# Performance work log

Measured on AMD Instinct MI355X. Metric: run time of the kernel, lower is better.

Reference implementation:

```python
import jax, jax.numpy as jnp
import numpy as np

B, N, C_IN, C_H, C_OUT, R, X_DIM = 32, 256, 64, 128, 128, 5, 1024
NEG = -9e15

def _leaky(x, s=0.2):
    return jnp.where(x >= 0, x, s * x)

def gat_layer(atoms, mask, W, b, a):
    # atoms: (B,n,c_in), mask: (B,n,n,R) bool, W: (c_in, R*c), b: (R*c,), a: (R, 2c)
    bs, n, _ = atoms.shape
    c = a.shape[1] // 2
    h = (atoms @ W + b).reshape(bs, n, R, c)            # (B,n,R,c)
    src = jnp.einsum('bnrc,rc->bnr', h, a[:, :c])       # a . h_i part
    dst = jnp.einsum('bnrc,rc->bnr', h, a[:, c:])       # a . h_j part
    logits = _leaky(src[:, :, None, :] + dst[:, None, :, :])  # (B,i,j,R)
    masked = jnp.where(mask, logits, NEG)
    probs = jax.nn.softmax(masked.reshape(bs, n, n * R), axis=2).reshape(bs, n, n, R)
    return jnp.einsum('bijr,bjrc->bic', probs, h)       # (B,n,c)

def setup_inputs() -> dict:
    key = jax.random.key(0)
    ks = jax.random.split(key, 16)
    def p(k, shape, fan):
        return jax.random.normal(k, shape, jnp.float32) * (1.414 / np.sqrt(fan))
    inp = {
        'x': jax.random.normal(ks[0], (B, X_DIM), jnp.float32),
        'y_atoms': jax.random.normal(ks[1], (B, N, C_IN), jnp.float32),
        'y_bonds': jax.random.randint(ks[2], (B, N, N, R), 0, 2, jnp.int32),
        'W1': p(ks[3], (C_IN, R * C_H), C_IN), 'b1': jnp.zeros((R * C_H,), jnp.float32),
        'a1': p(ks[4], (R, 2 * C_H), 2 * C_H),
        'W2': p(ks[5], (C_H, R * C_H), C_H), 'b2': jnp.zeros((R * C_H,), jnp.float32),
        'a2': p(ks[6], (R, 2 * C_H), 2 * C_H),
        'W3': p(ks[7], (C_H, R * C_OUT), C_H), 'b3': jnp.zeros((R * C_OUT,), jnp.float32),
        'a3': p(ks[8], (R, 2 * C_OUT), 2 * C_OUT),
        'We1': p(ks[9], (2 * C_OUT + X_DIM, 256), 2 * C_OUT + X_DIM), 'be1': jnp.zeros((256,), jnp.float32),
        'We2': p(ks[10], (256, 32), 256), 'be2': jnp.zeros((32,), jnp.float32),
        'We3': p(ks[11], (32, 1), 32), 'be3': jnp.zeros((1,), jnp.float32),
    }
    return inp

def reference(x, y_atoms, y_bonds, W1, b1, a1, W2, b2, a2, W3, b3, a3,
              We1, be1, We2, be2, We3, be3):
    mask = (y_bonds == 1)
    h = gat_layer(y_atoms, mask, W1, b1, a1)
    h = _leaky(h)                                   # dropout is identity at eval
    h = gat_layer(h, mask, W2, b2, a2)
    h = _leaky(h)
    h = gat_layer(h, mask, W3, b3, a3)
    y_feats = jnp.concatenate([jnp.mean(h, axis=1), jnp.max(h, axis=1)], axis=1)
    z = jnp.concatenate([x, y_feats], axis=1)
    z = _leaky(z @ We1 + be1)
    z = _leaky(z @ We2 + be2)
    return z @ We3 + be3
```

## Files before the change

### kernel.cpp

```cpp
#include <hip/hip_runtime.h>
#include <cstddef>

#define BB 32
#define NN 256
#define RR 5

typedef __attribute__((ext_vector_type(8))) short bf16x8;
typedef __attribute__((ext_vector_type(4))) float f32x4;

__device__ __forceinline__ float lrelu(float x) { return x >= 0.f ? x : 0.2f * x; }
__device__ __forceinline__ unsigned short f2bf(float x) {
    unsigned u = __float_as_uint(x);
    u += 0x7FFFu + ((u >> 16) & 1u);
    return (unsigned short)(u >> 16);
}
__device__ __forceinline__ float bf2f(unsigned short u) {
    return __uint_as_float((unsigned)u << 16);
}

__global__ __launch_bounds__(256) void k_prep(const float* __restrict__ W1,
                                              const float* __restrict__ W2,
                                              const float* __restrict__ W3,
                                              const int* __restrict__ bonds,
                                              unsigned short* __restrict__ WT1,
                                              unsigned short* __restrict__ WT2,
                                              unsigned short* __restrict__ WT3,
                                              unsigned char* __restrict__ maskp) {
    int blk = blockIdx.x;
    int t = threadIdx.x;
    if (blk < 30) {
        int layer = blk / 10, nt = blk % 10;
        const float* W;
        unsigned short* WT;
        int K;
        if (layer == 0)      { W = W1; WT = WT1; K = 64; }
        else if (layer == 1) { W = W2; WT = WT2; K = 128; }
        else                 { W = W3; WT = WT3; K = 128; }
        int n = nt * 64 + (t & 63);
        for (int kg = (int)(t >> 6); kg < K / 8; kg += 4) {
            bf16x8 v;
#pragma unroll
            for (int e = 0; e < 8; ++e) v[e] = (short)f2bf(W[(size_t)(kg * 8 + e) * 640 + n]);
            *(bf16x8*)&WT[(size_t)n * K + kg * 8] = v;
        }
    } else {
        int gt = (blk - 30) * 256 + t;
        const int4* p = (const int4*)(bonds + (size_t)gt * 20);
        int4 q0 = p[0], q1 = p[1], q2 = p[2], q3 = p[3], q4 = p[4];
        int v[20] = {q0.x, q0.y, q0.z, q0.w, q1.x, q1.y, q1.z, q1.w,
                     q2.x, q2.y, q2.z, q2.w, q3.x, q3.y, q3.z, q3.w,
                     q4.x, q4.y, q4.z, q4.w};
        unsigned m = 0;
#pragma unroll
        for (int k = 0; k < 4; ++k)
#pragma unroll
            for (int r = 0; r < 5; ++r)
                m |= (v[k * 5 + r] == 1) ? (1u << (k * 8 + r)) : 0u;
        *(unsigned*)&maskp[(size_t)gt * 4] = m;
    }
}

template <int K, int MODE>
__global__ __launch_bounds__(256) void k_gemm_h(const float* __restrict__ Af32,
                                                const unsigned short* __restrict__ Ab,
                                                const unsigned short* __restrict__ WTg,
                                                const float* __restrict__ bias,
                                                const float* __restrict__ avec,
                                                float* __restrict__ srcp,
                                                float* __restrict__ dstp,
                                                unsigned short* __restrict__ hTf) {
    const int t = threadIdx.x;
    const int l = blockIdx.x;
    const int mt = (l & 7) * 16 + ((l >> 3) & 15);
    const int nt = l >> 7;
    const int n0 = nt * 64, m0 = mt * 64;
    const int w = t >> 6, lane = t & 63;
    const int colg = lane & 15, rquad = lane >> 4;
    const int m = m0 + w * 16 + colg;
    const int koff = rquad * 8;

    f32x4 acc[4] = {};
#pragma unroll
    for (int kk = 0; kk < K; kk += 32) {
        bf16x8 af;
        size_t off = (size_t)m * K + kk + koff;
        if (MODE == 1) {
            af = *(const bf16x8*)&Ab[off];
        } else {
            float4 q0 = *(const float4*)&Af32[off];
            float4 q1 = *(const float4*)&Af32[off + 4];
            af[0] = (short)f2bf(q0.x); af[1] = (short)f2bf(q0.y);
            af[2] = (short)f2bf(q0.z); af[3] = (short)f2bf(q0.w);
            af[4] = (short)f2bf(q1.x); af[5] = (short)f2bf(q1.y);
            af[6] = (short)f2bf(q1.z); af[7] = (short)f2bf(q1.w);
        }
#pragma unroll
        for (int ct = 0; ct < 4; ++ct) {
            bf16x8 bfv = *(const bf16x8*)&WTg[(size_t)(n0 + ct * 16 + colg) * K + kk + koff];
            acc[ct] = __builtin_amdgcn_mfma_f32_16x16x32_bf16(af, bfv, acc[ct], 0, 0, 0);
        }
    }

    const int r = n0 >> 7, chalf = n0 & 127;
    const int b = m0 >> 8, jb = m0 & 255;
    float val[4][4];
    float ssum[4] = {0.f, 0.f, 0.f, 0.f}, dsum[4] = {0.f, 0.f, 0.f, 0.f};
#pragma unroll
    for (int ct = 0; ct < 4; ++ct) {
        int cg = chalf + ct * 16 + colg;
        float bv = bias[n0 + ct * 16 + colg];
        float asr = avec[r * 256 + cg];
        float ads = avec[r * 256 + 128 + cg];
#pragma unroll
        for (int reg = 0; reg < 4; ++reg) {
            float v = acc[ct][reg] + bv;
            val[ct][reg] = v;
            ssum[reg] += v * asr;
            dsum[reg] += v * ads;
        }
    }
#pragma unroll
    for (int mk = 1; mk < 16; mk <<= 1)
#pragma unroll
        for (int reg = 0; reg < 4; ++reg) {
            ssum[reg] += __shfl_xor(ssum[reg], mk);
            dsum[reg] += __shfl_xor(dsum[reg], mk);
        }
    if (colg == 0) {
        int half = (n0 >> 6) & 1;
#pragma unroll
        for (int reg = 0; reg < 4; ++reg) {
            int row = m0 + w * 16 + rquad * 4 + reg;
            srcp[half * 40960 + row * 5 + r] = ssum[reg];
            dstp[half * 40960 + row * 5 + r] = dsum[reg];
        }
    }
    {
        const int joct = (jb >> 3) + w * 2 + (rquad >> 1);
        const size_t tile = (size_t)((b * 5 + r) * 32 + joct) * 1024;
        const int sub = (rquad & 1) * 4;
#pragma unroll
        for (int ct = 0; ct < 4; ++ct) {
            int c = chalf + ct * 16 + colg;
            uint2 pk;
            pk.x = (unsigned)f2bf(val[ct][0]) | ((unsigned)f2bf(val[ct][1]) << 16);
            pk.y = (unsigned)f2bf(val[ct][2]) | ((unsigned)f2bf(val[ct][3]) << 16);
            *(uint2*)&hTf[tile + (size_t)c * 8 + sub] = pk;
        }
    }
}

template <int FINAL>
__global__ __launch_bounds__(512, 4) void k_agg(const unsigned short* __restrict__ hTf,
                                                const float* __restrict__ srcp,
                                                const float* __restrict__ dstp,
                                                const unsigned char* __restrict__ maskp,
                                                unsigned short* __restrict__ Ab,
                                                float* __restrict__ poolS,
                                                float* __restrict__ poolM) {
    __shared__ __align__(16) unsigned short Ps[20480];
    __shared__ __align__(16) float Ds2l[1280];
    __shared__ float Ss[80], Zw[128], Zrow[16];
    const int t = threadIdx.x;
    const int l = blockIdx.x;
    const int b = (l & 7) * 4 + ((l >> 3) & 3);
    const int itile = l >> 5;
    const int ib = b * 256 + itile * 16;
    const int w = t >> 6, lane = t & 63;
    const int colg = lane & 15, rquad = lane >> 4;
    const int c = w * 16 + colg;
    const size_t bbase = (size_t)(b * 5) * 32 * 1024;

    if (t < 80) Ss[t] = srcp[(size_t)ib * 5 + t] + srcp[40960 + (size_t)ib * 5 + t];
    for (int idx = t; idx < 1280; idx += 512) {
        int jl = idx & 255, rr = idx >> 8;
        size_t o = (size_t)(b * 256 + jl) * 5 + rr;
        Ds2l[rr * 256 + jl] = dstp[o] + dstp[40960 + o];
    }
    bf16x8 pre[4];
#pragma unroll
    for (int s = 0; s < 4; ++s)
        pre[s] = *(const bf16x8*)&hTf[bbase + (size_t)(s * 4 + rquad) * 1024 + (size_t)c * 8];
    __syncthreads();

    {
        const int i = t & 15;
        const int kq = (t >> 4) & 3;
        float esum = 0.f;
#pragma unroll
        for (int it = 0; it < 5; ++it) {
            int p = it * 512 + t;
            int s = p >> 6;
            int k0 = s * 32 + kq * 8;
            int rr = k0 >> 8, j0 = k0 & 255;
            uint2 mk8 = *(const uint2*)&maskp[((size_t)(ib + i) << 8) + j0];
            float sv = Ss[i * 5 + rr];
            float4 d0 = *(const float4*)&Ds2l[rr * 256 + j0];
            float4 d1 = *(const float4*)&Ds2l[rr * 256 + j0 + 4];
            float dv[8] = {d0.x, d0.y, d0.z, d0.w, d1.x, d1.y, d1.z, d1.w};
            bf16x8 pv;
#pragma unroll
            for (int e = 0; e < 8; ++e) {
                unsigned mb = ((e < 4 ? (mk8.x >> (8 * e)) : (mk8.y >> (8 * (e - 4)))) >> rr) & 1u;
                float vv = lrelu(sv + dv[e]);
                float ev = mb ? __expf(vv) : 0.f;
                unsigned short q = f2bf(ev);
                pv[e] = (short)q;
                esum += __uint_as_float((unsigned)q << 16);
            }
            *(bf16x8*)&Ps[p * 8] = pv;
        }
        esum += __shfl_xor(esum, 16);
        esum += __shfl_xor(esum, 32);
        if (lane < 16) Zw[w * 16 + (lane & 15)] = esum;
    }
    __syncthreads();
    if (t < 16) {
        float z = 0.f;
#pragma unroll
        for (int ww = 0; ww < 8; ++ww) z += Zw[ww * 16 + t];
        Zrow[t] = 1.f / z;
    }

    f32x4 acc0 = {}, acc1 = {};
#pragma unroll
    for (int s = 0; s < 8; ++s) {
        bf16x8 af = *(const bf16x8*)&Ps[(s * 64 + lane) * 8];
        bf16x8 bfv;
        if (s < 4) bfv = pre[s];
        else bfv = *(const bf16x8*)&hTf[bbase + (size_t)((s & 7) * 4 + rquad) * 1024 + (size_t)c * 8];
        if (s & 1) acc1 = __builtin_amdgcn_mfma_f32_16x16x32_bf16(af, bfv, acc1, 0, 0, 0);
        else       acc0 = __builtin_amdgcn_mfma_f32_16x16x32_bf16(af, bfv, acc0, 0, 0, 0);
    }
#pragma unroll 8
    for (int s = 8; s < 40; ++s) {
        bf16x8 af = *(const bf16x8*)&Ps[(s * 64 + lane) * 8];
        bf16x8 bfv = *(const bf16x8*)&hTf[bbase +
            (size_t)((s >> 3) * 32 + (s & 7) * 4 + rquad) * 1024 + (size_t)c * 8];
        if (s & 1) acc1 = __builtin_amdgcn_mfma_f32_16x16x32_bf16(af, bfv, acc1, 0, 0, 0);
        else       acc0 = __builtin_amdgcn_mfma_f32_16x16x32_bf16(af, bfv, acc0, 0, 0, 0);
    }
    __syncthreads();
    const int irow = ib + rquad * 4;
    if (FINAL) {
        float ps = 0.f, pm = -3.4e38f;
#pragma unroll
        for (int reg = 0; reg < 4; ++reg) {
            float v = (acc0[reg] + acc1[reg]) * Zrow[rquad * 4 + reg];
            ps += v;
            pm = fmaxf(pm, v);
        }
        ps += __shfl_xor(ps, 16);
        ps += __shfl_xor(ps, 32);
        pm = fmaxf(pm, __shfl_xor(pm, 16));
        pm = fmaxf(pm, __shfl_xor(pm, 32));
        if (rquad == 0) {
            poolS[(size_t)(b * 16 + itile) * 128 + c] = ps;
            poolM[(size_t)(b * 16 + itile) * 128 + c] = pm;
        }
    } else {
#pragma unroll
        for (int reg = 0; reg < 4; ++reg) {
            float v = (acc0[reg] + acc1[reg]) * Zrow[rquad * 4 + reg];
            Ab[(size_t)(irow + reg) * 128 + c] = f2bf(lrelu(v));
        }
    }
}

__global__ __launch_bounds__(256) void k_mlp1(const float* __restrict__ x,
                                              const float* __restrict__ poolS,
                                              const float* __restrict__ poolM,
                                              const float* __restrict__ We1,
                                              float* __restrict__ z1p) {
    const int kg = blockIdx.x, b = blockIdx.y;
    const int t = threadIdx.x;
    __shared__ float zs[256];
    if (kg < 4) {
        zs[t] = x[(size_t)b * 1024 + kg * 256 + t];
    } else if (t < 128) {
        float s = 0.f;
#pragma unroll
        for (int it = 0; it < 16; ++it) s += poolS[(size_t)(b * 16 + it) * 128 + t];
        zs[t] = s * (1.f / 256.f);
    } else {
        int f = t - 128;
        float mx = -3.4e38f;
#pragma unroll
        for (int it = 0; it < 16; ++it) mx = fmaxf(mx, poolM[(size_t)(b * 16 + it) * 128 + f]);
        zs[t] = mx;
    }
    __syncthreads();
    float s = 0.f;
#pragma unroll 8
    for (int k = 0; k < 256; ++k) s += zs[k] * We1[(size_t)(kg * 256 + k) * 256 + t];
    z1p[(size_t)(b * 5 + kg) * 256 + t] = s;
}

__global__ __launch_bounds__(256) void k_mlp2(const float* __restrict__ z1p,
                                              const float* __restrict__ be1,
                                              const float* __restrict__ We2,
                                              const float* __restrict__ be2,
                                              const float* __restrict__ We3,
                                              const float* __restrict__ be3,
                                              float* __restrict__ out) {
    const int b = blockIdx.x, t = threadIdx.x;
    __shared__ float z1s[256];
    __shared__ float s2p[8][32];
    __shared__ float z2s[32];
    {
        float s = be1[t];
#pragma unroll
        for (int kg = 0; kg < 5; ++kg) s += z1p[(size_t)(b * 5 + kg) * 256 + t];
        z1s[t] = lrelu(s);
    }
    __syncthreads();
    {
        int o = t & 31, g = t >> 5;
        float p = 0.f;
#pragma unroll
        for (int k = 0; k < 32; ++k) p += z1s[g * 32 + k] * We2[(g * 32 + k) * 32 + o];
        s2p[g][o] = p;
    }
    __syncthreads();
    if (t < 32) {
        float s2 = be2[t];
#pragma unroll
        for (int g = 0; g < 8; ++g) s2 += s2p[g][t];
        z2s[t] = lrelu(s2);
    }
    __syncthreads();
    if (t == 0) {
        float s3 = be3[0];
#pragma unroll
        for (int k = 0; k < 32; ++k) s3 += z2s[k] * We3[k];
        out[b] = s3;
    }
}

constexpr size_t O_MASK  = 0;
constexpr size_t O_SRCP  = 2097152;
constexpr size_t O_DSTP  = O_SRCP + 2ull * 40960 * 4;
constexpr size_t O_AB    = O_DSTP + 2ull * 40960 * 4;
constexpr size_t O_HT    = O_AB + 2097152;
constexpr size_t O_WT1   = O_HT + 5242880ull * 2;
constexpr size_t O_WT2   = O_WT1 + 640ull * 64 * 2;
constexpr size_t O_WT3   = O_WT2 + 640ull * 128 * 2;
constexpr size_t O_POOLS = O_WT3 + 640ull * 128 * 2;
constexpr size_t O_POOLM = O_POOLS + 32ull * 16 * 128 * 4;
constexpr size_t O_Z1P   = O_POOLM + 32ull * 16 * 128 * 4;

extern "C" void kernel_launch(void* const* d_in, const int* in_sizes, int n_in,
                              void* d_out, int out_size, void* d_ws, size_t ws_size,
                              hipStream_t stream) {
    const float* x       = (const float*)d_in[0];
    const float* y_atoms = (const float*)d_in[1];
    const int*   y_bonds = (const int*)d_in[2];
    const float* W1 = (const float*)d_in[3];
    const float* b1 = (const float*)d_in[4];
    const float* a1 = (const float*)d_in[5];
    const float* W2 = (const float*)d_in[6];
    const float* b2 = (const float*)d_in[7];
    const float* a2 = (const float*)d_in[8];
    const float* W3 = (const float*)d_in[9];
    const float* b3 = (const float*)d_in[10];
    const float* a3 = (const float*)d_in[11];
    const float* We1 = (const float*)d_in[12];
    const float* be1 = (const float*)d_in[13];
    const float* We2 = (const float*)d_in[14];
    const float* be2 = (const float*)d_in[15];
    const float* We3 = (const float*)d_in[16];
    const float* be3 = (const float*)d_in[17];
    float* out = (float*)d_out;

    char* ws = (char*)d_ws;
    unsigned char* maskp = (unsigned char*)(ws + O_MASK);
    float* srcp = (float*)(ws + O_SRCP);
    float* dstp = (float*)(ws + O_DSTP);
    unsigned short* Ab = (unsigned short*)(ws + O_AB);
    unsigned short* hTf = (unsigned short*)(ws + O_HT);
    unsigned short* WT1 = (unsigned short*)(ws + O_WT1);
    unsigned short* WT2 = (unsigned short*)(ws + O_WT2);
    unsigned short* WT3 = (unsigned short*)(ws + O_WT3);
    float* poolS = (float*)(ws + O_POOLS);
    float* poolM = (float*)(ws + O_POOLM);
    float* z1p   = (float*)(ws + O_Z1P);

    dim3 blk(256);

    k_prep<<<2078, blk, 0, stream>>>(W1, W2, W3, y_bonds, WT1, WT2, WT3, maskp);

    k_gemm_h<64, 0><<<1280, blk, 0, stream>>>(
        y_atoms, nullptr, WT1, b1, a1, srcp, dstp, hTf);
    k_agg<0><<<512, dim3(512), 0, stream>>>(hTf, srcp, dstp, maskp, Ab, nullptr, nullptr);

    k_gemm_h<128, 1><<<1280, blk, 0, stream>>>(
        nullptr, Ab, WT2, b2, a2, srcp, dstp, hTf);
    k_agg<0><<<512, dim3(512), 0, stream>>>(hTf, srcp, dstp, maskp, Ab, nullptr, nullptr);

    k_gemm_h<128, 1><<<1280, blk, 0, stream>>>(
        nullptr, Ab, WT3, b3, a3, srcp, dstp, hTf);
    k_agg<1><<<512, dim3(512), 0, stream>>>(hTf, srcp, dstp, maskp, nullptr, poolS, poolM);

    k_mlp1<<<dim3(5, 32), blk, 0, stream>>>(x, poolS, poolM, We1, z1p);
    k_mlp2<<<32, blk, 0, stream>>>(z1p, be1, We2, be2, We3, be3, out);
}
```

Measured before the change: 202.1 us.

## Fuse all stages into one persistent kernel with atomic grid barriers

Replaces the nine separate launches (prep, three GEMM/aggregation pairs, two MLP stages) with a single persistent kernel of 512 blocks of 512 threads. Stages are separated by software grid barriers built on an atomic counter. Each block runs two 256-thread GEMM sub-tiles at once, and the W2/W3 transposes and mask packing are overlapped with the first GEMM stage. The aim is to remove per-launch overhead and tail gaps between kernels. In exchange it adds barrier spin cost and a memset, and it depends on all 512 blocks being co-resident, otherwise it deadlocks.

```diff
diff --git a/kernel.cpp b/kernel.cpp
--- a/kernel.cpp
+++ b/kernel.cpp
@@ -1,9 +1,7 @@
 #include <hip/hip_runtime.h>
 #include <cstddef>
 
-#define BB 32
-#define NN 256
-#define RR 5
+#define NBLK 512
 
 typedef __attribute__((ext_vector_type(8))) short bf16x8;
 typedef __attribute__((ext_vector_type(4))) float f32x4;
@@ -18,59 +16,56 @@
     return __uint_as_float((unsigned)u << 16);
 }
 
-__global__ __launch_bounds__(256) void k_prep(const float* __restrict__ W1,
-                                              const float* __restrict__ W2,
-                                              const float* __restrict__ W3,
-                                              const int* __restrict__ bonds,
-                                              unsigned short* __restrict__ WT1,
-                                              unsigned short* __restrict__ WT2,
-                                              unsigned short* __restrict__ WT3,
-                                              unsigned char* __restrict__ maskp) {
-    int blk = blockIdx.x;
-    int t = threadIdx.x;
-    if (blk < 30) {
-        int layer = blk / 10, nt = blk % 10;
-        const float* W;
-        unsigned short* WT;
-        int K;
-        if (layer == 0)      { W = W1; WT = WT1; K = 64; }
-        else if (layer == 1) { W = W2; WT = WT2; K = 128; }
-        else                 { W = W3; WT = WT3; K = 128; }
-        int n = nt * 64 + (t & 63);
-        for (int kg = (int)(t >> 6); kg < K / 8; kg += 4) {
-            bf16x8 v;
-#pragma unroll
-            for (int e = 0; e < 8; ++e) v[e] = (short)f2bf(W[(size_t)(kg * 8 + e) * 640 + n]);
-            *(bf16x8*)&WT[(size_t)n * K + kg * 8] = v;
-        }
-    } else {
-        int gt = (blk - 30) * 256 + t;
-        const int4* p = (const int4*)(bonds + (size_t)gt * 20);
-        int4 q0 = p[0], q1 = p[1], q2 = p[2], q3 = p[3], q4 = p[4];
-        int v[20] = {q0.x, q0.y, q0.z, q0.w, q1.x, q1.y, q1.z, q1.w,
-                     q2.x, q2.y, q2.z, q2.w, q3.x, q3.y, q3.z, q3.w,
-                     q4.x, q4.y, q4.z, q4.w};
-        unsigned m = 0;
-#pragma unroll
-        for (int k = 0; k < 4; ++k)
-#pragma unroll
-            for (int r = 0; r < 5; ++r)
-                m |= (v[k * 5 + r] == 1) ? (1u << (k * 8 + r)) : 0u;
-        *(unsigned*)&maskp[(size_t)gt * 4] = m;
-    }
+__device__ __forceinline__ void gbar(unsigned* bar, unsigned target) {
+    __syncthreads();
+    if (threadIdx.x == 0) {
+        __threadfence();
+        __hip_atomic_fetch_add(bar, 1u, __ATOMIC_RELAXED, __HIP_MEMORY_SCOPE_AGENT);
+        while (__hip_atomic_load(bar, __ATOMIC_RELAXED, __HIP_MEMORY_SCOPE_AGENT) < target)
+            __builtin_amdgcn_s_sleep(8);
+        __threadfence();
+    }
+    __syncthreads();
+}
+
+__device__ __forceinline__ void wtrans(const float* __restrict__ W,
+                                       unsigned short* __restrict__ WT,
+                                       int K, int nt, int t) {
+    int n = nt * 64 + (t & 63);
+    for (int kg = t >> 6; kg < K / 8; kg += 8) {
+        bf16x8 v;
+#pragma unroll
+        for (int e = 0; e < 8; ++e) v[e] = (short)f2bf(W[(size_t)(kg * 8 + e) * 640 + n]);
+        *(bf16x8*)&WT[(size_t)n * K + kg * 8] = v;
+    }
+}
+
+__device__ __forceinline__ void maskpack(const int* __restrict__ bonds,
+                                         unsigned char* __restrict__ maskp, int gt) {
+    const int4* p = (const int4*)(bonds + (size_t)gt * 20);
+    int4 q0 = p[0], q1 = p[1], q2 = p[2], q3 = p[3], q4 = p[4];
+    int v[20] = {q0.x, q0.y, q0.z, q0.w, q1.x, q1.y, q1.z, q1.w,
+                 q2.x, q2.y, q2.z, q2.w, q3.x, q3.y, q3.z, q3.w,
+                 q4.x, q4.y, q4.z, q4.w};
+    unsigned m = 0;
+#pragma unroll
+    for (int k = 0; k < 4; ++k)
+#pragma unroll
+        for (int r = 0; r < 5; ++r)
+            m |= (v[k * 5 + r] == 1) ? (1u << (k * 8 + r)) : 0u;
+    *(unsigned*)&maskp[(size_t)gt * 4] = m;
 }
 
 template <int K, int MODE>
-__global__ __launch_bounds__(256) void k_gemm_h(const float* __restrict__ Af32,
-                                                const unsigned short* __restrict__ Ab,
-                                                const unsigned short* __restrict__ WTg,
-                                                const float* __restrict__ bias,
-                                                const float* __restrict__ avec,
-                                                float* __restrict__ srcp,
-                                                float* __restrict__ dstp,
-                                                unsigned short* __restrict__ hTf) {
-    const int t = threadIdx.x;
-    const int l = blockIdx.x;
+__device__ __forceinline__ void gemm_body(int l, int t,
+                                          const float* __restrict__ Af32,
+                                          const unsigned short* __restrict__ Ab,
+                                          const unsigned short* __restrict__ WTg,
+                                          const float* __restrict__ bias,
+                                          const float* __restrict__ avec,
+                                          float* __restrict__ srcp,
+                                          float* __restrict__ dstp,
+                                          unsigned short* __restrict__ hTf) {
     const int mt = (l & 7) * 16 + ((l >> 3) & 15);
     const int nt = l >> 7;
     const int n0 = nt * 64, m0 = mt * 64;
@@ -127,12 +122,12 @@
             dsum[reg] += __shfl_xor(dsum[reg], mk);
         }
     if (colg == 0) {
-        int half = (n0 >> 6) & 1;
+        int nhalf = (n0 >> 6) & 1;
 #pragma unroll
         for (int reg = 0; reg < 4; ++reg) {
             int row = m0 + w * 16 + rquad * 4 + reg;
-            srcp[half * 40960 + row * 5 + r] = ssum[reg];
-            dstp[half * 40960 + row * 5 + r] = dsum[reg];
+            srcp[nhalf * 40960 + row * 5 + r] = ssum[reg];
+            dstp[nhalf * 40960 + row * 5 + r] = dsum[reg];
         }
     }
     {
@@ -151,18 +146,20 @@
 }
 
 template <int FINAL>
-__global__ __launch_bounds__(512, 4) void k_agg(const unsigned short* __restrict__ hTf,
-                                                const float* __restrict__ srcp,
-                                                const float* __restrict__ dstp,
-                                                const unsigned char* __restrict__ maskp,
-                                                unsigned short* __restrict__ Ab,
-                                                float* __restrict__ poolS,
-                                                float* __restrict__ poolM) {
-    __shared__ __align__(16) unsigned short Ps[20480];
-    __shared__ __align__(16) float Ds2l[1280];
-    __shared__ float Ss[80], Zw[128], Zrow[16];
-    const int t = threadIdx.x;
-    const int l = blockIdx.x;
+__device__ __forceinline__ void agg_body(int l, int t, unsigned char* SM,
+                                         const unsigned short* __restrict__ hTf,
+                                         const float* __restrict__ srcp,
+                                         const float* __restrict__ dstp,
+                                         const unsigned char* __restrict__ maskp,
+                                         unsigned short* __restrict__ Ab,
+                                         float* __restrict__ poolS,
+                                         float* __restrict__ poolM) {
+    unsigned short* Ps = (unsigned short*)SM;
+    float* Ds2l = (float*)(SM + 40960);
+    float* Ss   = (float*)(SM + 46080);
+    float* Zw   = (float*)(SM + 46400);
+    float* Zrow = (float*)(SM + 46912);
+
     const int b = (l & 7) * 4 + ((l >> 3) & 3);
     const int itile = l >> 5;
     const int ib = b * 256 + itile * 16;
@@ -267,14 +264,13 @@
     }
 }
 
-__global__ __launch_bounds__(256) void k_mlp1(const float* __restrict__ x,
-                                              const float* __restrict__ poolS,
-                                              const float* __restrict__ poolM,
-                                              const float* __restrict__ We1,
-                                              float* __restrict__ z1p) {
-    const int kg = blockIdx.x, b = blockIdx.y;
-    const int t = threadIdx.x;
-    __shared__ float zs[256];
+__device__ __forceinline__ void mlp1_body(int vb, int t, float* zs,
+                                          const float* __restrict__ x,
+                                          const float* __restrict__ poolS,
+                                          const float* __restrict__ poolM,
+                                          const float* __restrict__ We1,
+                                          float* __restrict__ z1p) {
+    const int kg = vb % 5, b = vb / 5;
     if (kg < 4) {
         zs[t] = x[(size_t)b * 1024 + kg * 256 + t];
     } else if (t < 128) {
@@ -296,36 +292,36 @@
     z1p[(size_t)(b * 5 + kg) * 256 + t] = s;
 }
 
-__global__ __launch_bounds__(256) void k_mlp2(const float* __restrict__ z1p,
-                                              const float* __restrict__ be1,
-                                              const float* __restrict__ We2,
-                                              const float* __restrict__ be2,
-                                              const float* __restrict__ We3,
-                                              const float* __restrict__ be3,
-                                              float* __restrict__ out) {
-    const int b = blockIdx.x, t = threadIdx.x;
-    __shared__ float z1s[256];
-    __shared__ float s2p[8][32];
-    __shared__ float z2s[32];
-    {
+__device__ __forceinline__ void mlp2_body(int b, int t, unsigned char* SM,
+                                          const float* __restrict__ z1p,
+                                          const float* __restrict__ be1,
+                                          const float* __restrict__ We2,
+                                          const float* __restrict__ be2,
+                                          const float* __restrict__ We3,
+                                          const float* __restrict__ be3,
+                                          float* __restrict__ out) {
+    float* z1s = (float*)SM;
+    float* s2p = (float*)(SM + 1024);
+    float* z2s = (float*)(SM + 2048);
+    if (t < 256) {
         float s = be1[t];
 #pragma unroll
         for (int kg = 0; kg < 5; ++kg) s += z1p[(size_t)(b * 5 + kg) * 256 + t];
         z1s[t] = lrelu(s);
     }
     __syncthreads();
-    {
+    if (t < 256) {
         int o = t & 31, g = t >> 5;
         float p = 0.f;
 #pragma unroll
         for (int k = 0; k < 32; ++k) p += z1s[g * 32 + k] * We2[(g * 32 + k) * 32 + o];
-        s2p[g][o] = p;
+        s2p[g * 32 + o] = p;
     }
     __syncthreads();
     if (t < 32) {
         float s2 = be2[t];
 #pragma unroll
-        for (int g = 0; g < 8; ++g) s2 += s2p[g][t];
+        for (int g = 0; g < 8; ++g) s2 += s2p[g * 32 + t];
         z2s[t] = lrelu(s2);
     }
     __syncthreads();
@@ -337,17 +333,75 @@
     }
 }
 
+__global__ __launch_bounds__(512, 4) void k_mega(
+    const float* __restrict__ x, const float* __restrict__ y_atoms,
+    const int* __restrict__ bonds,
+    const float* __restrict__ W1, const float* __restrict__ b1, const float* __restrict__ a1,
+    const float* __restrict__ W2, const float* __restrict__ b2, const float* __restrict__ a2,
+    const float* __restrict__ W3, const float* __restrict__ b3, const float* __restrict__ a3,
+    const float* __restrict__ We1, const float* __restrict__ be1,
+    const float* __restrict__ We2, const float* __restrict__ be2,
+    const float* __restrict__ We3, const float* __restrict__ be3,
+    unsigned char* __restrict__ maskp, float* __restrict__ srcp, float* __restrict__ dstp,
+    unsigned short* __restrict__ Ab, unsigned short* __restrict__ hTf,
+    unsigned short* __restrict__ WT1, unsigned short* __restrict__ WT2,
+    unsigned short* __restrict__ WT3,
+    float* __restrict__ poolS, float* __restrict__ poolM, float* __restrict__ z1p,
+    unsigned* bar, float* __restrict__ out) {
+    __shared__ __align__(16) unsigned char SM[46976];
+    const int rb = blockIdx.x;
+    const int t = threadIdx.x;
+    const int hb = t >> 8, t2 = t & 255;
+
+    if (rb < 10) wtrans(W1, WT1, 64, rb, t);
+    gbar(bar, NBLK * 1);
+
+    for (int vb = rb * 2 + hb; vb < 1280; vb += 1024)
+        gemm_body<64, 0>(vb, t2, y_atoms, nullptr, WT1, b1, a1, srcp, dstp, hTf);
+    if (rb >= 480 && rb < 490)      wtrans(W2, WT2, 128, rb - 480, t);
+    else if (rb >= 490 && rb < 500) wtrans(W3, WT3, 128, rb - 490, t);
+    {
+        int gt = rb * 512 + t;
+        maskpack(bonds, maskp, gt);
+        maskpack(bonds, maskp, gt + 262144);
+    }
+    gbar(bar, NBLK * 2);
+
+    agg_body<0>(rb, t, SM, hTf, srcp, dstp, maskp, Ab, nullptr, nullptr);
+    gbar(bar, NBLK * 3);
+
+    for (int vb = rb * 2 + hb; vb < 1280; vb += 1024)
+        gemm_body<128, 1>(vb, t2, nullptr, Ab, WT2, b2, a2, srcp, dstp, hTf);
+    gbar(bar, NBLK * 4);
+
+    agg_body<0>(rb, t, SM, hTf, srcp, dstp, maskp, Ab, nullptr, nullptr);
+    gbar(bar, NBLK * 5);
+
+    for (int vb = rb * 2 + hb; vb < 1280; vb += 1024)
+        gemm_body<128, 1>(vb, t2, nullptr, Ab, WT3, b3, a3, srcp, dstp, hTf);
+    gbar(bar, NBLK * 6);
+
+    agg_body<1>(rb, t, SM, hTf, srcp, dstp, maskp, nullptr, poolS, poolM);
+    gbar(bar, NBLK * 7);
+
+    if (rb < 80) mlp1_body(rb * 2 + hb, t2, (float*)(SM + hb * 1024), x, poolS, poolM, We1, z1p);
+    gbar(bar, NBLK * 8);
+
+    if (rb < 32) mlp2_body(rb, t, SM, z1p, be1, We2, be2, We3, be3, out);
+}
+
 constexpr size_t O_MASK  = 0;
 constexpr size_t O_SRCP  = 2097152;
-constexpr size_t O_DSTP  = O_SRCP + 2ull * 40960 * 4;
-constexpr size_t O_AB    = O_DSTP + 2ull * 40960 * 4;
+constexpr size_t O_DSTP  = O_SRCP + 327680;
+constexpr size_t O_AB    = O_DSTP + 327680;
 constexpr size_t O_HT    = O_AB + 2097152;
-constexpr size_t O_WT1   = O_HT + 5242880ull * 2;
-constexpr size_t O_WT2   = O_WT1 + 640ull * 64 * 2;
-constexpr size_t O_WT3   = O_WT2 + 640ull * 128 * 2;
-constexpr size_t O_POOLS = O_WT3 + 640ull * 128 * 2;
-constexpr size_t O_POOLM = O_POOLS + 32ull * 16 * 128 * 4;
-constexpr size_t O_Z1P   = O_POOLM + 32ull * 16 * 128 * 4;
+constexpr size_t O_WT1   = O_HT + 10485760;
+constexpr size_t O_WT2   = O_WT1 + 81920;
+constexpr size_t O_WT3   = O_WT2 + 163840;
+constexpr size_t O_POOLS = O_WT3 + 163840;
+constexpr size_t O_POOLM = O_POOLS + 262144;
+constexpr size_t O_Z1P   = O_POOLM + 262144;
+constexpr size_t O_BAR   = O_Z1P + 163840;
 
 extern "C" void kernel_launch(void* const* d_in, const int* in_sizes, int n_in,
                               void* d_out, int out_size, void* d_ws, size_t ws_size,
@@ -384,23 +438,11 @@
     float* poolS = (float*)(ws + O_POOLS);
     float* poolM = (float*)(ws + O_POOLM);
     float* z1p   = (float*)(ws + O_Z1P);
-
-    dim3 blk(256);
-
-    k_prep<<<2078, blk, 0, stream>>>(W1, W2, W3, y_bonds, WT1, WT2, WT3, maskp);
-
-    k_gemm_h<64, 0><<<1280, blk, 0, stream>>>(
-        y_atoms, nullptr, WT1, b1, a1, srcp, dstp, hTf);
-    k_agg<0><<<512, dim3(512), 0, stream>>>(hTf, srcp, dstp, maskp, Ab, nullptr, nullptr);
-
-    k_gemm_h<128, 1><<<1280, blk, 0, stream>>>(
-        nullptr, Ab, WT2, b2, a2, srcp, dstp, hTf);
-    k_agg<0><<<512, dim3(512), 0, stream>>>(hTf, srcp, dstp, maskp, Ab, nullptr, nullptr);
-
-    k_gemm_h<128, 1><<<1280, blk, 0, stream>>>(
-        nullptr, Ab, WT3, b3, a3, srcp, dstp, hTf);
-    k_agg<1><<<512, dim3(512), 0, stream>>>(hTf, srcp, dstp, maskp, nullptr, poolS, poolM);
-
-    k_mlp1<<<dim3(5, 32), blk, 0, stream>>>(x, poolS, poolM, We1, z1p);
-    k_mlp2<<<32, blk, 0, stream>>>(z1p, be1, We2, be2, We3, be3, out);
-}
+    unsigned* bar = (unsigned*)(ws + O_BAR);
+
+    hipMemsetAsync(bar, 0, 64, stream);
+    k_mega<<<NBLK, 512, 0, stream>>>(
+        x, y_atoms, y_bonds, W1, b1, a1, W2, b2, a2, W3, b3, a3,
+        We1, be1, We2, be2, We3, be3,
+        maskp, srcp, dstp, Ab, hTf, WT1, WT2, WT3, poolS, poolM, z1p, bar, out);
+}
```

After: 635.2 us. 3.14x slower.

## Fold mask and W2/W3 prep into first GEMM launch; merge MLP kernels

Applied to the files above, without the earlier changes.

Splits the prep kernel so only the W1 transpose stays as a small standalone launch. Mask packing and the W2/W3 bf16 transposes now run as extra blocks appended to the first GEMM launch, so they overlap with layer-1 GEMM work. The two MLP kernels are merged into one tail kernel that does the full 1280-wide We1 reduction per batch row. This removes launches and the z1p round-trip, but the tail now runs only 32 blocks, each with a longer serial loop.

```diff
diff --git a/kernel.cpp b/kernel.cpp
--- a/kernel.cpp
+++ b/kernel.cpp
@@ -1,9 +1,5 @@
 #include <hip/hip_runtime.h>
 #include <cstddef>
-
-#define BB 32
-#define NN 256
-#define RR 5
 
 typedef __attribute__((ext_vector_type(8))) short bf16x8;
 typedef __attribute__((ext_vector_type(4))) float f32x4;
@@ -14,53 +10,20 @@
     u += 0x7FFFu + ((u >> 16) & 1u);
     return (unsigned short)(u >> 16);
 }
-__device__ __forceinline__ float bf2f(unsigned short u) {
-    return __uint_as_float((unsigned)u << 16);
-}
-
-__global__ __launch_bounds__(256) void k_prep(const float* __restrict__ W1,
-                                              const float* __restrict__ W2,
-                                              const float* __restrict__ W3,
-                                              const int* __restrict__ bonds,
-                                              unsigned short* __restrict__ WT1,
-                                              unsigned short* __restrict__ WT2,
-                                              unsigned short* __restrict__ WT3,
-                                              unsigned char* __restrict__ maskp) {
-    int blk = blockIdx.x;
-    int t = threadIdx.x;
-    if (blk < 30) {
-        int layer = blk / 10, nt = blk % 10;
-        const float* W;
-        unsigned short* WT;
-        int K;
-        if (layer == 0)      { W = W1; WT = WT1; K = 64; }
-        else if (layer == 1) { W = W2; WT = WT2; K = 128; }
-        else                 { W = W3; WT = WT3; K = 128; }
-        int n = nt * 64 + (t & 63);
-        for (int kg = (int)(t >> 6); kg < K / 8; kg += 4) {
-            bf16x8 v;
-#pragma unroll
-            for (int e = 0; e < 8; ++e) v[e] = (short)f2bf(W[(size_t)(kg * 8 + e) * 640 + n]);
-            *(bf16x8*)&WT[(size_t)n * K + kg * 8] = v;
-        }
-    } else {
-        int gt = (blk - 30) * 256 + t;
-        const int4* p = (const int4*)(bonds + (size_t)gt * 20);
-        int4 q0 = p[0], q1 = p[1], q2 = p[2], q3 = p[3], q4 = p[4];
-        int v[20] = {q0.x, q0.y, q0.z, q0.w, q1.x, q1.y, q1.z, q1.w,
-                     q2.x, q2.y, q2.z, q2.w, q3.x, q3.y, q3.z, q3.w,
-                     q4.x, q4.y, q4.z, q4.w};
-        unsigned m = 0;
-#pragma unroll
-        for (int k = 0; k < 4; ++k)
-#pragma unroll
-            for (int r = 0; r < 5; ++r)
-                m |= (v[k * 5 + r] == 1) ? (1u << (k * 8 + r)) : 0u;
-        *(unsigned*)&maskp[(size_t)gt * 4] = m;
-    }
-}
-
-template <int K, int MODE>
+
+__global__ __launch_bounds__(256) void k_prepw(const float* __restrict__ W1,
+                                               unsigned short* __restrict__ WT1) {
+    const int nt = blockIdx.x, t = threadIdx.x;
+    const int n = nt * 64 + (t & 63);
+    for (int kg = t >> 6; kg < 8; kg += 4) {
+        bf16x8 v;
+#pragma unroll
+        for (int e = 0; e < 8; ++e) v[e] = (short)f2bf(W1[(size_t)(kg * 8 + e) * 640 + n]);
+        *(bf16x8*)&WT1[(size_t)n * 64 + kg * 8] = v;
+    }
+}
+
+template <int K, int MODE, int EXTRA>
 __global__ __launch_bounds__(256) void k_gemm_h(const float* __restrict__ Af32,
                                                 const unsigned short* __restrict__ Ab,
                                                 const unsigned short* __restrict__ WTg,
@@ -68,9 +31,47 @@
                                                 const float* __restrict__ avec,
                                                 float* __restrict__ srcp,
                                                 float* __restrict__ dstp,
-                                                unsigned short* __restrict__ hTf) {
+                                                unsigned short* __restrict__ hTf,
+                                                const int* __restrict__ bonds,
+                                                unsigned char* __restrict__ maskp,
+                                                const float* __restrict__ W2,
+                                                const float* __restrict__ W3,
+                                                unsigned short* __restrict__ WT2,
+                                                unsigned short* __restrict__ WT3) {
     const int t = threadIdx.x;
     const int l = blockIdx.x;
+    if (EXTRA && l >= 1280) {
+        int e = l - 1280;
+        if (e < 2048) {
+            int gt = e * 256 + t;
+            const int4* p = (const int4*)(bonds + (size_t)gt * 20);
+            int4 q0 = p[0], q1 = p[1], q2 = p[2], q3 = p[3], q4 = p[4];
+            int v[20] = {q0.x, q0.y, q0.z, q0.w, q1.x, q1.y, q1.z, q1.w,
+                         q2.x, q2.y, q2.z, q2.w, q3.x, q3.y, q3.z, q3.w,
+                         q4.x, q4.y, q4.z, q4.w};
+            unsigned m = 0;
+#pragma unroll
+            for (int k = 0; k < 4; ++k)
+#pragma unroll
+                for (int r = 0; r < 5; ++r)
+                    m |= (v[k * 5 + r] == 1) ? (1u << (k * 8 + r)) : 0u;
+            *(unsigned*)&maskp[(size_t)gt * 4] = m;
+        } else {
+            int e2 = e - 2048;
+            const float* W = (e2 < 10) ? W2 : W3;
+            unsigned short* WT = (e2 < 10) ? WT2 : WT3;
+            int nt = (e2 < 10) ? e2 : e2 - 10;
+            int n = nt * 64 + (t & 63);
+            for (int kg = t >> 6; kg < 16; kg += 4) {
+                bf16x8 v;
+#pragma unroll
+                for (int ee = 0; ee < 8; ++ee)
+                    v[ee] = (short)f2bf(W[(size_t)(kg * 8 + ee) * 640 + n]);
+                *(bf16x8*)&WT[(size_t)n * 128 + kg * 8] = v;
+            }
+        }
+        return;
+    }
     const int mt = (l & 7) * 16 + ((l >> 3) & 15);
     const int nt = l >> 7;
     const int n0 = nt * 64, m0 = mt * 64;
@@ -127,12 +128,12 @@
             dsum[reg] += __shfl_xor(dsum[reg], mk);
         }
     if (colg == 0) {
-        int half = (n0 >> 6) & 1;
+        int nhalf = (n0 >> 6) & 1;
 #pragma unroll
         for (int reg = 0; reg < 4; ++reg) {
             int row = m0 + w * 16 + rquad * 4 + reg;
-            srcp[half * 40960 + row * 5 + r] = ssum[reg];
-            dstp[half * 40960 + row * 5 + r] = dsum[reg];
+            srcp[nhalf * 40960 + row * 5 + r] = ssum[reg];
+            dstp[nhalf * 40960 + row * 5 + r] = dsum[reg];
         }
     }
     {
@@ -267,50 +268,39 @@
     }
 }
 
-__global__ __launch_bounds__(256) void k_mlp1(const float* __restrict__ x,
+__global__ __launch_bounds__(256) void k_tail(const float* __restrict__ x,
                                               const float* __restrict__ poolS,
                                               const float* __restrict__ poolM,
                                               const float* __restrict__ We1,
-                                              float* __restrict__ z1p) {
-    const int kg = blockIdx.x, b = blockIdx.y;
-    const int t = threadIdx.x;
-    __shared__ float zs[256];
-    if (kg < 4) {
-        zs[t] = x[(size_t)b * 1024 + kg * 256 + t];
-    } else if (t < 128) {
-        float s = 0.f;
-#pragma unroll
-        for (int it = 0; it < 16; ++it) s += poolS[(size_t)(b * 16 + it) * 128 + t];
-        zs[t] = s * (1.f / 256.f);
-    } else {
-        int f = t - 128;
-        float mx = -3.4e38f;
-#pragma unroll
-        for (int it = 0; it < 16; ++it) mx = fmaxf(mx, poolM[(size_t)(b * 16 + it) * 128 + f]);
-        zs[t] = mx;
-    }
-    __syncthreads();
-    float s = 0.f;
-#pragma unroll 8
-    for (int k = 0; k < 256; ++k) s += zs[k] * We1[(size_t)(kg * 256 + k) * 256 + t];
-    z1p[(size_t)(b * 5 + kg) * 256 + t] = s;
-}
-
-__global__ __launch_bounds__(256) void k_mlp2(const float* __restrict__ z1p,
                                               const float* __restrict__ be1,
                                               const float* __restrict__ We2,
                                               const float* __restrict__ be2,
                                               const float* __restrict__ We3,
                                               const float* __restrict__ be3,
                                               float* __restrict__ out) {
-    const int b = blockIdx.x, t = threadIdx.x;
+    __shared__ float zs[1280];
     __shared__ float z1s[256];
     __shared__ float s2p[8][32];
     __shared__ float z2s[32];
+    const int b = blockIdx.x, t = threadIdx.x;
+    for (int k = t; k < 1024; k += 256) zs[k] = x[(size_t)b * 1024 + k];
+    if (t < 128) {
+        float s = 0.f;
+#pragma unroll
+        for (int it = 0; it < 16; ++it) s += poolS[(size_t)(b * 16 + it) * 128 + t];
+        zs[1024 + t] = s * (1.f / 256.f);
+    } else {
+        int f = t - 128;
+        float mx = -3.4e38f;
+#pragma unroll
+        for (int it = 0; it < 16; ++it) mx = fmaxf(mx, poolM[(size_t)(b * 16 + it) * 128 + f]);
+        zs[1152 + f] = mx;
+    }
+    __syncthreads();
     {
         float s = be1[t];
-#pragma unroll
-        for (int kg = 0; kg < 5; ++kg) s += z1p[(size_t)(b * 5 + kg) * 256 + t];
+#pragma unroll 8
+        for (int k = 0; k < 1280; ++k) s += zs[k] * We1[(size_t)k * 256 + t];
         z1s[t] = lrelu(s);
     }
     __syncthreads();
@@ -347,7 +337,6 @@
 constexpr size_t O_WT3   = O_WT2 + 640ull * 128 * 2;
 constexpr size_t O_POOLS = O_WT3 + 640ull * 128 * 2;
 constexpr size_t O_POOLM = O_POOLS + 32ull * 16 * 128 * 4;
-constexpr size_t O_Z1P   = O_POOLM + 32ull * 16 * 128 * 4;
 
 extern "C" void kernel_launch(void* const* d_in, const int* in_sizes, int n_in,
                               void* d_out, int out_size, void* d_ws, size_t ws_size,
@@ -383,24 +372,25 @@
     unsigned short* WT3 = (unsigned short*)(ws + O_WT3);
     float* poolS = (float*)(ws + O_POOLS);
     float* poolM = (float*)(ws + O_POOLM);
-    float* z1p   = (float*)(ws + O_Z1P);
 
     dim3 blk(256);
 
-    k_prep<<<2078, blk, 0, stream>>>(W1, W2, W3, y_bonds, WT1, WT2, WT3, maskp);
-
-    k_gemm_h<64, 0><<<1280, blk, 0, stream>>>(
-        y_atoms, nullptr, WT1, b1, a1, srcp, dstp, hTf);
+    k_prepw<<<10, blk, 0, stream>>>(W1, WT1);
+
+    k_gemm_h<64, 0, 1><<<3348, blk, 0, stream>>>(
+        y_atoms, nullptr, WT1, b1, a1, srcp, dstp, hTf,
+        y_bonds, maskp, W2, W3, WT2, WT3);
     k_agg<0><<<512, dim3(512), 0, stream>>>(hTf, srcp, dstp, maskp, Ab, nullptr, nullptr);
 
-    k_gemm_h<128, 1><<<1280, blk, 0, stream>>>(
-        nullptr, Ab, WT2, b2, a2, srcp, dstp, hTf);
+    k_gemm_h<128, 1, 0><<<1280, blk, 0, stream>>>(
+        nullptr, Ab, WT2, b2, a2, srcp, dstp, hTf,
+        nullptr, nullptr, nullptr, nullptr, nullptr, nullptr);
     k_agg<0><<<512, dim3(512), 0, stream>>>(hTf, srcp, dstp, maskp, Ab, nullptr, nullptr);
 
-    k_gemm_h<128, 1><<<1280, blk, 0, stream>>>(
-        nullptr, Ab, WT3, b3, a3, srcp, dstp, hTf);
+    k_gemm_h<128, 1, 0><<<1280, blk, 0, stream>>>(
+        nullptr, Ab, WT3, b3, a3, srcp, dstp, hTf,
+        nullptr, nullptr, nullptr, nullptr, nullptr, nullptr);
     k_agg<1><<<512, dim3(512), 0, stream>>>(hTf, srcp, dstp, maskp, nullptr, poolS, poolM);
 
-    k_mlp1<<<dim3(5, 32), blk, 0, stream>>>(x, poolS, poolM, We1, z1p);
-    k_mlp2<<<32, blk, 0, stream>>>(z1p, be1, We2, be2, We3, be3, out);
-}
+    k_tail<<<32, blk, 0, stream>>>(x, poolS, poolM, We1, be1, We2, be2, We3, be3, out);
+}
```

Result: slower. 233.5 us (+15.5%).
